# Performance work log

Hardware: AMD Instinct MI355X
Metric: run time of the kernel (lower is better)

## Reference

```python
import jax, jax.numpy as jnp
import numpy as np
from jax import lax

B, H, W = 32, 80, 80
K = 100                        # max_candidates
THRESH = 0.1                   # minutiae_threshold
DIST_T = 16.0
ANGLE_T = np.pi / 6.0
PI = np.pi


def _gauss_kernel1d(ks, sigma):
    c = jnp.arange(ks, dtype=jnp.float32) - ks // 2
    g = jnp.exp(-(c * c) / (2.0 * sigma * sigma))
    return g / g.sum()


def _gaussian_blur(img):  # [B,1,H,W], separable 5x5 sigma=1.5
    k = _gauss_kernel1d(5, 1.5)
    dn = ('NCHW', 'OIHW', 'NCHW')
    x = lax.conv_general_dilated(img, k.reshape(1, 1, 1, 5), (1, 1), [(0, 0), (2, 2)], dimension_numbers=dn)
    x = lax.conv_general_dilated(x, k.reshape(1, 1, 5, 1), (1, 1), [(2, 2), (0, 0)], dimension_numbers=dn)
    return x


def _up8(m):  # nearest-neighbor x8 upsample on last two dims
    return jnp.repeat(jnp.repeat(m, 8, axis=-2), 8, axis=-1)


def _detect_and_nms(score, ori, xoff, yoff):
    # score [H,W]; ori [90,H,W]; xoff/yoff [8,H,W]
    vals, idx = lax.top_k(score.reshape(-1), K)   # sorted descending == argsort by score
    valid = vals > THRESH
    rows = idx // W
    cols = idx % W
    ang_idx = jnp.argmax(ori[:, rows, cols], axis=0)   # [K]
    xo = jnp.argmax(xoff[:, rows, cols], axis=0)
    yo = jnp.argmax(yoff[:, rows, cols], axis=0)
    angles = (ang_idx.astype(jnp.float32) * 2.0 - 89.0) * (PI / 180.0)
    x = cols.astype(jnp.float32) * 8.0 + xo.astype(jnp.float32)
    y = rows.astype(jnp.float32) * 8.0 + yo.astype(jnp.float32)
    mnt = jnp.stack([x, y, angles, vals], axis=-1)     # [K,4]
    # pairwise suppression mask (cdist + circular angle delta)
    d2 = jnp.sum((mnt[:, None, :2] - mnt[None, :, :2]) ** 2, axis=-1)
    dist = jnp.sqrt(d2)
    ad = jnp.abs(angles[:, None] - angles[None, :])
    am = jnp.minimum(ad, 2.0 * PI - ad)
    sup = (dist < DIST_T) & (am < ANGLE_T)
    ar = jnp.arange(K)
    def body(i, keep):
        s = sup[i] & (ar > i)
        return jnp.where(keep[i], keep & ~s, keep)
    keep = lax.fori_loop(0, K, body, valid)
    return mnt, keep


def setup_inputs() -> dict:
    key = jax.random.key(0)
    ks = jax.random.split(key, 7)
    return {
        'segmentation': jax.random.uniform(ks[0], (B, 1, H, W), jnp.float32),
        'minutiae_score': jax.random.uniform(ks[1], (B, 1, H, W), jnp.float32),
        'minutiae_orientation': jax.random.normal(ks[2], (B, 90, H, W), jnp.float32),
        'minutiae_x_offset': jax.random.normal(ks[3], (B, 8, H, W), jnp.float32),
        'minutiae_y_offset': jax.random.normal(ks[4], (B, 8, H, W), jnp.float32),
        'orientation': jax.random.normal(ks[5], (B, 90, H, W), jnp.float32),
        'enhanced_real': jax.random.normal(ks[6], (B, 1, 8 * H, 8 * W), jnp.float32),
    }


def reference(segmentation, minutiae_score, minutiae_orientation,
              minutiae_x_offset, minutiae_y_offset, orientation, enhanced_real):
    # --- segmentation mask: round -> gaussian blur -> round
    cleaned = jnp.round(_gaussian_blur(jnp.round(segmentation[:, 0])[:, None]))[:, 0]  # [B,H,W]
    cleaned_up = _up8(cleaned)                                                          # [B,8H,8W]
    # --- minutiae detection (threshold via masked top-k) + sequential NMS
    score = minutiae_score[:, 0] * cleaned
    mnt, keep = jax.vmap(_detect_and_nms)(score, minutiae_orientation,
                                          minutiae_x_offset, minutiae_y_offset)
    # --- orientation field
    ori_idx = jnp.argmax(orientation, axis=1).astype(jnp.float32)   # [B,H,W]
    ori_field = (_up8(ori_idx) * 2.0 - 89.0) * (PI / 180.0) * cleaned_up
    # --- enhanced image: mask + per-image min-max normalize to [0,255]
    enh = enhanced_real[:, 0] * cleaned_up
    ef = enh.reshape(B, -1)
    emin = jnp.min(ef, axis=1, keepdims=True)
    emax = jnp.max(ef, axis=1, keepdims=True)
    enorm = (ef - emin) / (emax - emin + 1e-8)
    enh_visual = enorm.reshape(B, 8 * H, 8 * W) * 255.0
    return (mnt, keep.astype(jnp.float32), enh_visual, cleaned_up * 255.0, ori_field)
```

## Files before the change

kernel.cpp:

```cpp
#include <hip/hip_runtime.h>
#include <math.h>

#define BN  32
#define H   80
#define W   80
#define HW  6400
#define KC  100
#define NCH 90
#define UW  640
#define UHW 409600

static constexpr size_t OUT_MNT   = 0;
static constexpr size_t OUT_KEEP  = (size_t)BN * KC * 4;
static constexpr size_t OUT_ENH   = OUT_KEEP + (size_t)BN * KC;
static constexpr size_t OUT_CLEAN = OUT_ENH + (size_t)BN * UHW;
static constexpr size_t OUT_ORI   = OUT_CLEAN + (size_t)BN * UHW;

#define PI_F 3.14159265358979323846
#define MM_BLOCKS 64
#define CAP 2048
#define CLEAN_BLOCKS 320
#define ORI_BLOCKS2 400
#define GAT_BLOCKS 800
#define FIN_BLOCKS 12800

typedef float vfloat4 __attribute__((ext_vector_type(4)));

__device__ __forceinline__ unsigned enc_f(float f) {
    unsigned u = __float_as_uint(f);
    return (u & 0x80000000u) ? ~u : (u | 0x80000000u);
}
__device__ __forceinline__ float dec_f(unsigned k) {
    return (k & 0x80000000u) ? __uint_as_float(k ^ 0x80000000u) : __uint_as_float(~k);
}
__device__ __forceinline__ unsigned long long shflx(unsigned long long v, int off) {
    unsigned hi = (unsigned)__shfl_xor((int)(unsigned)(v >> 32), off);
    unsigned lo = (unsigned)__shfl_xor((int)(unsigned)(v & 0xffffffffull), off);
    return ((unsigned long long)hi << 32) | lo;
}

__global__ __launch_bounds__(512) void k_pre(const float* __restrict__ seg,
                                             const float* __restrict__ ori,
                                             float* __restrict__ cleaned_g,
                                             float* __restrict__ ori_idx) {
    __shared__ __align__(16) char um[16384];
    const int bx = blockIdx.x, tid = threadIdx.x;

    if (bx < CLEAN_BLOCKS) {
        float* s_in = (float*)um;
        float* s_h  = (float*)um + 960;
        const int b = bx / 10, band = bx % 10;
        const int r0 = band * 8 - 2;

        float g[5];
        {
            float s = 0.f;
            #pragma unroll
            for (int i = 0; i < 5; i++) {
                float c = (float)(i - 2);
                g[i] = expf(-(c * c) / 4.5f);
                s += g[i];
            }
            #pragma unroll
            for (int i = 0; i < 5; i++) g[i] /= s;
        }

        for (int i = tid; i < 12 * 80; i += 512) {
            int lr = i / 80, w = i % 80;
            int gr = r0 + lr;
            s_in[i] = (gr >= 0 && gr < H) ? rintf(seg[(size_t)b * HW + gr * W + w]) : 0.f;
        }
        __syncthreads();
        for (int i = tid; i < 12 * 80; i += 512) {
            int lr = i / 80, w = i % 80;
            float acc = 0.f;
            #pragma unroll
            for (int dx = -2; dx <= 2; dx++) {
                int ww = w + dx;
                if (ww >= 0 && ww < W) acc += s_in[lr * 80 + ww] * g[dx + 2];
            }
            s_h[i] = acc;
        }
        __syncthreads();
        for (int i = tid; i < 8 * 80; i += 512) {
            int k = i / 80, w = i % 80;
            float acc = 0.f;
            #pragma unroll
            for (int dy = 0; dy < 5; dy++) acc += s_h[(k + dy) * 80 + w] * g[dy];
            cleaned_g[(size_t)b * HW + (band * 8 + k) * W + w] = rintf(acc);
        }
    } else {
        float4* s_bv = (float4*)um;
        float4* s_bj = (float4*)um + 512;
        const int grp = tid >> 7, ln = tid & 127;
        const int p4 = (bx - CLEAN_BLOCKS) * 128 + ln;
        const int b = p4 / (HW / 4), pp = p4 % (HW / 4);
        const float4* o = (const float4*)(ori + (size_t)b * NCH * HW) + pp;
        const int cs = (grp * NCH) >> 2, ce = ((grp + 1) * NCH) >> 2;

        float4 bv = o[(size_t)cs * (HW / 4)];
        float4 bj = make_float4((float)cs, (float)cs, (float)cs, (float)cs);
        for (int j = cs + 1; j < ce; j++) {
            float4 v = o[(size_t)j * (HW / 4)];
            if (v.x > bv.x) { bv.x = v.x; bj.x = (float)j; }
            if (v.y > bv.y) { bv.y = v.y; bj.y = (float)j; }
            if (v.z > bv.z) { bv.z = v.z; bj.z = (float)j; }
            if (v.w > bv.w) { bv.w = v.w; bj.w = (float)j; }
        }
        s_bv[tid] = bv; s_bj[tid] = bj;
        __syncthreads();
        if (grp == 0) {
            #pragma unroll
            for (int g = 1; g < 4; g++) {
                float4 v = s_bv[g * 128 + ln], jx = s_bj[g * 128 + ln];
                if (v.x > bv.x) { bv.x = v.x; bj.x = jx.x; }
                if (v.y > bv.y) { bv.y = v.y; bj.y = jx.y; }
                if (v.z > bv.z) { bv.z = v.z; bj.z = jx.z; }
                if (v.w > bv.w) { bv.w = v.w; bj.w = jx.w; }
            }
            ((float4*)ori_idx)[p4] = bj;
        }
    }
}

__global__ __launch_bounds__(512) void k_mid(const float* __restrict__ mscore,
                                             const float* __restrict__ cleaned,
                                             const float* __restrict__ enh,
                                             float* __restrict__ pmin,
                                             float* __restrict__ pmax,
                                             int* __restrict__ ws_idx,
                                             float* __restrict__ ws_val) {
    __shared__ __align__(16) char um[20480];
    __shared__ unsigned long long s_sel[KC];
    __shared__ unsigned s_rm[HW / 32];
    __shared__ int s_cnt[5];
    __shared__ int s_n;
    __shared__ float s_T;
    __shared__ int s_mode;
    __shared__ float smin[8], smax[8];

    const int bx = blockIdx.x, tid = threadIdx.x;
    const int lane = tid & 63;

    if (bx < BN) {
        unsigned long long* s_cand = (unsigned long long*)um;
        unsigned long long* s_red  = (unsigned long long*)um + CAP;
        const int b = bx;

        if (tid < HW / 32) s_rm[tid] = 0u;
        if (tid < 5) s_cnt[tid] = 0;
        __syncthreads();

        float sc[13];
        #pragma unroll
        for (int j = 0; j < 13; j++) {
            int i = j * 512 + tid;
            sc[j] = (i < HW) ? mscore[(size_t)b * HW + i] * cleaned[(size_t)b * HW + i]
                             : -1.0f;
        }

        int c0 = 0, c1 = 0, c2 = 0, c3 = 0, c4 = 0;
        #pragma unroll
        for (int j = 0; j < 13; j++) {
            float v = sc[j];
            c0 += (v > 0.95f); c1 += (v > 0.9f); c2 += (v > 0.8f);
            c3 += (v > 0.5f);  c4 += (v > 0.0f);
        }
        #pragma unroll
        for (int off = 32; off > 0; off >>= 1) {
            c0 += __shfl_xor(c0, off); c1 += __shfl_xor(c1, off);
            c2 += __shfl_xor(c2, off); c3 += __shfl_xor(c3, off);
            c4 += __shfl_xor(c4, off);
        }
        if (lane == 0) {
            atomicAdd(&s_cnt[0], c0); atomicAdd(&s_cnt[1], c1);
            atomicAdd(&s_cnt[2], c2); atomicAdd(&s_cnt[3], c3);
            atomicAdd(&s_cnt[4], c4);
        }
        __syncthreads();

        if (tid == 0) {
            int n95 = s_cnt[0], n90 = s_cnt[1], n80 = s_cnt[2], n50 = s_cnt[3], n0 = s_cnt[4];
            int mode; float T = 0.f;
            if (n0 < KC)                      { mode = 1; }
            else if (n95 >= KC && n95 <= CAP) { mode = 0; T = 0.95f; }
            else if (n90 >= KC && n90 <= CAP) { mode = 0; T = 0.9f; }
            else if (n80 >= KC && n80 <= CAP) { mode = 0; T = 0.8f; }
            else if (n50 >= KC && n50 <= CAP) { mode = 0; T = 0.5f; }
            else if (n0 <= CAP)               { mode = 0; T = 0.0f; }
            else                              { mode = 2; }
            s_mode = mode; s_T = T; s_n = 0;
        }
        __syncthreads();
        const int mode = s_mode;

        if (mode != 2) {
            const float T = s_T;
            #pragma unroll
            for (int j = 0; j < 13; j++) {
                int i = j * 512 + tid;
                bool take = (mode == 0) ? (sc[j] > T)
                                        : (sc[j] > 0.f || (i < 256 && sc[j] == 0.0f));
                if (take) {
                    int pos = atomicAdd(&s_n, 1);
                    s_cand[pos] = ((unsigned long long)enc_f(sc[j]) << 32) | (unsigned)(HW - i);
                }
            }
            __syncthreads();
            const int n = s_n;
            for (int c = tid; c < n; c += 512) {
                unsigned long long kk = s_cand[c];
                int rank = 0;
                for (int m = 0; m < n; m++) rank += (s_cand[m] > kk) ? 1 : 0;
                if (rank < KC) s_sel[rank] = kk;
            }
            __syncthreads();
        } else {
            for (int k = 0; k < KC; k++) {
                unsigned long long lmax = 0ull;
                #pragma unroll
                for (int j = 0; j < 13; j++) {
                    int i = j * 512 + tid;
                    if (i < HW && sc[j] >= 0.f && !((s_rm[i >> 5] >> (i & 31)) & 1u)) {
                        unsigned long long kk =
                            ((unsigned long long)enc_f(sc[j]) << 32) | (unsigned)(HW - i);
                        if (kk > lmax) lmax = kk;
                    }
                }
                s_red[tid] = lmax;
                __syncthreads();
                for (int off = 256; off > 0; off >>= 1) {
                    if (tid < off) {
                        unsigned long long o = s_red[tid + off];
                        if (o > s_red[tid]) s_red[tid] = o;
                    }
                    __syncthreads();
                }
                if (tid == 0) {
                    unsigned long long wkey = s_red[0];
                    s_sel[k] = wkey;
                    int wi = HW - (int)(wkey & 0xffffffffull);
                    s_rm[wi >> 5] |= 1u << (wi & 31);
                }
                __syncthreads();
            }
        }

        if (tid < KC) {
            unsigned long long e = s_sel[tid];
            ws_idx[(size_t)b * KC + tid] = HW - (int)(e & 0xffffffffull);
            ws_val[(size_t)b * KC + tid] = dec_f((unsigned)(e >> 32));
        }
    } else {
        const int mb = bx - BN;
        const int b = mb >> 6, chunk = mb & 63;
        const float4* e4 = (const float4*)(enh + (size_t)b * UHW);
        const float* cb = cleaned + (size_t)b * HW;

        float vmin = INFINITY, vmax = -INFINITY;
        for (int i = chunk * 512 + tid; i < UHW / 4; i += MM_BLOCKS * 512) {
            float4 v = e4[i];
            int p = i * 4;
            int Y = p / UW, X = p % UW;
            float c = cb[(Y >> 3) * W + (X >> 3)];
            float a = v.x * c, bb = v.y * c, cc = v.z * c, dd = v.w * c;
            vmin = fminf(vmin, fminf(fminf(a, bb), fminf(cc, dd)));
            vmax = fmaxf(vmax, fmaxf(fmaxf(a, bb), fmaxf(cc, dd)));
        }
        #pragma unroll
        for (int off = 32; off > 0; off >>= 1) {
            vmin = fminf(vmin, __shfl_xor(vmin, off));
            vmax = fmaxf(vmax, __shfl_xor(vmax, off));
        }
        int wave = tid >> 6;
        if (lane == 0) { smin[wave] = vmin; smax[wave] = vmax; }
        __syncthreads();
        if (tid == 0) {
            float m0 = smin[0], m1 = smax[0];
            #pragma unroll
            for (int wv = 1; wv < 8; wv++) {
                m0 = fminf(m0, smin[wv]);
                m1 = fmaxf(m1, smax[wv]);
            }
            pmin[b * MM_BLOCKS + chunk] = m0;
            pmax[b * MM_BLOCKS + chunk] = m1;
        }
    }
}

__global__ __launch_bounds__(256) void k_fg(const float* __restrict__ enh,
                                            const float* __restrict__ cleaned,
                                            const float* __restrict__ ori_idx,
                                            const float* __restrict__ pmin,
                                            const float* __restrict__ pmax,
                                            const float* __restrict__ mori,
                                            const float* __restrict__ mxo,
                                            const float* __restrict__ myo,
                                            const int* __restrict__ ws_idx,
                                            const float* __restrict__ ws_val,
                                            float* __restrict__ out) {
    const int bx = blockIdx.x, tid = threadIdx.x;

    if (bx < GAT_BLOCKS) {
        const int lane = tid & 63;
        const int wid = bx * 4 + (tid >> 6);
        const int b = wid / KC, k = wid % KC;
        const int idx = ws_idx[(size_t)b * KC + k];

        const float* pm = mori + (size_t)b * NCH * HW + idx;
        unsigned long long kk =
            ((unsigned long long)enc_f(pm[(size_t)lane * HW]) << 32) | (unsigned)(127 - lane);
        if (lane < NCH - 64) {
            unsigned long long k1 =
                ((unsigned long long)enc_f(pm[(size_t)(64 + lane) * HW]) << 32)
                | (unsigned)(127 - (64 + lane));
            if (k1 > kk) kk = k1;
        }
        unsigned long long kx = 0ull, ky = 0ull;
        if (lane >= 32 && lane < 40)
            kx = ((unsigned long long)enc_f(mxo[((size_t)b * 8 + (lane - 32)) * HW + idx]) << 32)
                 | (unsigned)(15 - (lane - 32));
        if (lane >= 40 && lane < 48)
            ky = ((unsigned long long)enc_f(myo[((size_t)b * 8 + (lane - 40)) * HW + idx]) << 32)
                 | (unsigned)(15 - (lane - 40));

        #pragma unroll
        for (int off = 32; off > 0; off >>= 1) {
            unsigned long long o;
            o = shflx(kk, off); if (o > kk) kk = o;
            o = shflx(kx, off); if (o > kx) kx = o;
            o = shflx(ky, off); if (o > ky) ky = o;
        }

        if (lane == 0) {
            int ch = 127 - (int)(kk & 0xffffffffull);
            int xo = 15  - (int)(kx & 0xffffffffull);
            int yo = 15  - (int)(ky & 0xffffffffull);
            int r = idx / W, c = idx % W;
            float4 m;
            m.x = (float)c * 8.0f + (float)xo;
            m.y = (float)r * 8.0f + (float)yo;
            m.z = ((float)ch * 2.0f - 89.0f) * (float)(PI_F / 180.0);
            m.w = ws_val[(size_t)b * KC + k];
            ((float4*)(out + OUT_MNT))[(size_t)b * KC + k] = m;
        }
    } else {
        __shared__ float s_emin, s_emax;
        const int fb = bx - GAT_BLOCKS;
        const int b = fb / 400;
        if (tid < 64) {
            float vmin = pmin[b * MM_BLOCKS + tid];
            float vmax = pmax[b * MM_BLOCKS + tid];
            #pragma unroll
            for (int off = 32; off > 0; off >>= 1) {
                vmin = fminf(vmin, __shfl_xor(vmin, off));
                vmax = fmaxf(vmax, __shfl_xor(vmax, off));
            }
            if (tid == 0) { s_emin = vmin; s_emax = vmax; }
        }
        __syncthreads();

        int t4 = fb * 256 + tid;
        int p4 = t4 % (UHW / 4);
        int p = p4 * 4;
        int Y = p / UW, X = p % UW;
        int cidx = b * HW + (Y >> 3) * W + (X >> 3);
        float c  = cleaned[cidx];
        float oi = ori_idx[cidx];
        float emin = s_emin, emax = s_emax;
        float inv = 255.0f / (emax - emin + 1e-8f);

        float4 e = ((const float4*)enh)[t4];
        vfloat4 ev;
        ev.x = (e.x * c - emin) * inv;
        ev.y = (e.y * c - emin) * inv;
        ev.z = (e.z * c - emin) * inv;
        ev.w = (e.w * c - emin) * inv;

        float cv = c * 255.0f;
        float ov = (oi * 2.0f - 89.0f) * (float)(PI_F / 180.0) * c;
        vfloat4 cvv = {cv, cv, cv, cv};
        vfloat4 ovv = {ov, ov, ov, ov};

        __builtin_nontemporal_store(ev,  ((vfloat4*)(out + OUT_ENH))   + t4);
        __builtin_nontemporal_store(cvv, ((vfloat4*)(out + OUT_CLEAN)) + t4);
        __builtin_nontemporal_store(ovv, ((vfloat4*)(out + OUT_ORI))   + t4);
    }
}

__global__ __launch_bounds__(64) void k_nms(float* __restrict__ out) {
    const int b = blockIdx.x, l = threadIdx.x;
    const float4* mnt = (const float4*)(out + OUT_MNT) + (size_t)b * KC;
    float4 m0 = mnt[l];
    bool has1 = (l + 64) < KC;
    float4 m1 = has1 ? mnt[l + 64] : make_float4(0.f, 0.f, 0.f, -1.f);
    int keep0 = (m0.w > 0.1f) ? 1 : 0;
    int keep1 = (has1 && m1.w > 0.1f) ? 1 : 0;

    for (int i = 0; i < KC; i++) {
        bool hi = i >= 64;
        int src = i & 63;
        float xi = __shfl(hi ? m1.x : m0.x, src);
        float yi = __shfl(hi ? m1.y : m0.y, src);
        float ai = __shfl(hi ? m1.z : m0.z, src);
        int   ki = __shfl(hi ? keep1 : keep0, src);
        if (ki) {
            if (keep0 && l > i) {
                float dx = xi - m0.x, dy = yi - m0.y;
                float dist = sqrtf(dx * dx + dy * dy);
                float ad = fabsf(ai - m0.z);
                float am = fminf(ad, (float)(2.0 * PI_F) - ad);
                if (dist < 16.0f && am < (float)(PI_F / 6.0)) keep0 = 0;
            }
            if (keep1 && (l + 64) > i) {
                float dx = xi - m1.x, dy = yi - m1.y;
                float dist = sqrtf(dx * dx + dy * dy);
                float ad = fabsf(ai - m1.z);
                float am = fminf(ad, (float)(2.0 * PI_F) - ad);
                if (dist < 16.0f && am < (float)(PI_F / 6.0)) keep1 = 0;
            }
        }
    }
    out[OUT_KEEP + (size_t)b * KC + l] = (float)keep0;
    if (has1) out[OUT_KEEP + (size_t)b * KC + 64 + l] = (float)keep1;
}

extern "C" void kernel_launch(void* const* d_in, const int* in_sizes, int n_in,
                              void* d_out, int out_size, void* d_ws, size_t ws_size,
                              hipStream_t stream) {
    const float* seg    = (const float*)d_in[0];
    const float* mscore = (const float*)d_in[1];
    const float* mori   = (const float*)d_in[2];
    const float* mxo    = (const float*)d_in[3];
    const float* myo    = (const float*)d_in[4];
    const float* ori    = (const float*)d_in[5];
    const float* enh    = (const float*)d_in[6];
    float* out = (float*)d_out;

    float* cleaned = (float*)d_ws;
    float* ori_idx = cleaned + (size_t)BN * HW;
    float* pmin    = ori_idx + (size_t)BN * HW;
    float* pmax    = pmin + (size_t)BN * MM_BLOCKS;
    int*   ws_idx  = (int*)(pmax + (size_t)BN * MM_BLOCKS);
    float* ws_val  = (float*)(ws_idx + (size_t)BN * KC);

    const int nPre = CLEAN_BLOCKS + ORI_BLOCKS2;
    const int nMid = BN + BN * MM_BLOCKS;
    const int nFG  = GAT_BLOCKS + FIN_BLOCKS;

    k_pre<<<nPre, 512, 0, stream>>>(seg, ori, cleaned, ori_idx);
    k_mid<<<nMid, 512, 0, stream>>>(mscore, cleaned, enh, pmin, pmax, ws_idx, ws_val);
    k_fg<<<nFG, 256, 0, stream>>>(enh, cleaned, ori_idx, pmin, pmax,
                                  mori, mxo, myo, ws_idx, ws_val, out);
    k_nms<<<BN, 64, 0, stream>>>(out);
}
```

Measured before the change: 94.07 us.

## Move cleaned/orientation output writes into mid kernel and finalize min/max via last-block

Moves the writes of the upsampled cleaned mask and orientation field out of the final kernel and into the middle kernel as extra blocks. These blocks can then run alongside the serial top-k selection blocks instead of waiting behind them. The per-image min/max reduction is finished by the last arriving block, detected with an atomic counter and threadfence, so the final kernel reads two scalars instead of re-reducing partials. This adds an atomic counter that must be reset each launch, and the middle kernel now launches more blocks.

```diff
diff --git a/kernel.cpp b/kernel.cpp
--- a/kernel.cpp
+++ b/kernel.cpp
@@ -21,8 +21,9 @@
 #define CAP 2048
 #define CLEAN_BLOCKS 320
 #define ORI_BLOCKS2 400
+#define FINA_BLOCKS 6400
 #define GAT_BLOCKS 800
-#define FIN_BLOCKS 12800
+#define FINB_BLOCKS 12800
 
 typedef float vfloat4 __attribute__((ext_vector_type(4)));
 
@@ -42,9 +43,12 @@
 __global__ __launch_bounds__(512) void k_pre(const float* __restrict__ seg,
                                              const float* __restrict__ ori,
                                              float* __restrict__ cleaned_g,
-                                             float* __restrict__ ori_idx) {
+                                             float* __restrict__ ori_idx,
+                                             int* __restrict__ cnt) {
     __shared__ __align__(16) char um[16384];
     const int bx = blockIdx.x, tid = threadIdx.x;
+
+    if (bx == 0 && tid < BN) cnt[tid] = 0;
 
     if (bx < CLEAN_BLOCKS) {
         float* s_in = (float*)um;
@@ -126,10 +130,14 @@
 __global__ __launch_bounds__(512) void k_mid(const float* __restrict__ mscore,
                                              const float* __restrict__ cleaned,
                                              const float* __restrict__ enh,
+                                             const float* __restrict__ ori_idx,
                                              float* __restrict__ pmin,
                                              float* __restrict__ pmax,
+                                             float* __restrict__ mm,
+                                             int* __restrict__ cnt,
                                              int* __restrict__ ws_idx,
-                                             float* __restrict__ ws_val) {
+                                             float* __restrict__ ws_val,
+                                             float* __restrict__ out) {
     __shared__ __align__(16) char um[20480];
     __shared__ unsigned long long s_sel[KC];
     __shared__ unsigned s_rm[HW / 32];
@@ -138,6 +146,7 @@
     __shared__ float s_T;
     __shared__ int s_mode;
     __shared__ float smin[8], smax[8];
+    __shared__ int s_last;
 
     const int bx = blockIdx.x, tid = threadIdx.x;
     const int lane = tid & 63;
@@ -251,7 +260,7 @@
             ws_idx[(size_t)b * KC + tid] = HW - (int)(e & 0xffffffffull);
             ws_val[(size_t)b * KC + tid] = dec_f((unsigned)(e >> 32));
         }
-    } else {
+    } else if (bx < BN + BN * MM_BLOCKS) {
         const int mb = bx - BN;
         const int b = mb >> 6, chunk = mb & 63;
         const float4* e4 = (const float4*)(enh + (size_t)b * UHW);
@@ -284,15 +293,46 @@
             }
             pmin[b * MM_BLOCKS + chunk] = m0;
             pmax[b * MM_BLOCKS + chunk] = m1;
-        }
+            __threadfence();
+            int done = atomicAdd(&cnt[b], 1);
+            s_last = (done == MM_BLOCKS - 1) ? 1 : 0;
+        }
+        __syncthreads();
+        if (s_last) {
+            __threadfence();
+            if (tid < MM_BLOCKS) {
+                float fmin = pmin[b * MM_BLOCKS + tid];
+                float fmax = pmax[b * MM_BLOCKS + tid];
+                #pragma unroll
+                for (int off = 32; off > 0; off >>= 1) {
+                    fmin = fminf(fmin, __shfl_xor(fmin, off));
+                    fmax = fmaxf(fmax, __shfl_xor(fmax, off));
+                }
+                if (tid == 0) { mm[2 * b] = fmin; mm[2 * b + 1] = fmax; }
+            }
+        }
+    } else {
+        const int fb = bx - (BN + BN * MM_BLOCKS);
+        const int t4 = fb * 512 + tid;
+        const int b = t4 / (UHW / 4);
+        const int p4 = t4 % (UHW / 4);
+        const int p = p4 * 4;
+        const int Y = p / UW, X = p % UW;
+        const int cidx = b * HW + (Y >> 3) * W + (X >> 3);
+        const float c  = cleaned[cidx];
+        const float oi = ori_idx[cidx];
+        const float cv = c * 255.0f;
+        const float ov = (oi * 2.0f - 89.0f) * (float)(PI_F / 180.0) * c;
+        vfloat4 cvv = {cv, cv, cv, cv};
+        vfloat4 ovv = {ov, ov, ov, ov};
+        __builtin_nontemporal_store(cvv, ((vfloat4*)(out + OUT_CLEAN)) + t4);
+        __builtin_nontemporal_store(ovv, ((vfloat4*)(out + OUT_ORI))   + t4);
     }
 }
 
 __global__ __launch_bounds__(256) void k_fg(const float* __restrict__ enh,
                                             const float* __restrict__ cleaned,
-                                            const float* __restrict__ ori_idx,
-                                            const float* __restrict__ pmin,
-                                            const float* __restrict__ pmax,
+                                            const float* __restrict__ mm,
                                             const float* __restrict__ mori,
                                             const float* __restrict__ mxo,
                                             const float* __restrict__ myo,
@@ -345,30 +385,17 @@
             ((float4*)(out + OUT_MNT))[(size_t)b * KC + k] = m;
         }
     } else {
-        __shared__ float s_emin, s_emax;
         const int fb = bx - GAT_BLOCKS;
+        const int t4 = fb * 256 + tid;
         const int b = fb / 400;
-        if (tid < 64) {
-            float vmin = pmin[b * MM_BLOCKS + tid];
-            float vmax = pmax[b * MM_BLOCKS + tid];
-            #pragma unroll
-            for (int off = 32; off > 0; off >>= 1) {
-                vmin = fminf(vmin, __shfl_xor(vmin, off));
-                vmax = fmaxf(vmax, __shfl_xor(vmax, off));
-            }
-            if (tid == 0) { s_emin = vmin; s_emax = vmax; }
-        }
-        __syncthreads();
-
-        int t4 = fb * 256 + tid;
-        int p4 = t4 % (UHW / 4);
-        int p = p4 * 4;
-        int Y = p / UW, X = p % UW;
-        int cidx = b * HW + (Y >> 3) * W + (X >> 3);
-        float c  = cleaned[cidx];
-        float oi = ori_idx[cidx];
-        float emin = s_emin, emax = s_emax;
-        float inv = 255.0f / (emax - emin + 1e-8f);
+        const int p4 = t4 % (UHW / 4);
+        const int p = p4 * 4;
+        const int Y = p / UW, X = p % UW;
+        const int cidx = b * HW + (Y >> 3) * W + (X >> 3);
+        const float c = cleaned[cidx];
+        const float emin = mm[2 * b];
+        const float emax = mm[2 * b + 1];
+        const float inv = 255.0f / (emax - emin + 1e-8f);
 
         float4 e = ((const float4*)enh)[t4];
         vfloat4 ev;
@@ -376,15 +403,7 @@
         ev.y = (e.y * c - emin) * inv;
         ev.z = (e.z * c - emin) * inv;
         ev.w = (e.w * c - emin) * inv;
-
-        float cv = c * 255.0f;
-        float ov = (oi * 2.0f - 89.0f) * (float)(PI_F / 180.0) * c;
-        vfloat4 cvv = {cv, cv, cv, cv};
-        vfloat4 ovv = {ov, ov, ov, ov};
-
-        __builtin_nontemporal_store(ev,  ((vfloat4*)(out + OUT_ENH))   + t4);
-        __builtin_nontemporal_store(cvv, ((vfloat4*)(out + OUT_CLEAN)) + t4);
-        __builtin_nontemporal_store(ovv, ((vfloat4*)(out + OUT_ORI))   + t4);
+        __builtin_nontemporal_store(ev, ((vfloat4*)(out + OUT_ENH)) + t4);
     }
 }
 
@@ -441,16 +460,19 @@
     float* ori_idx = cleaned + (size_t)BN * HW;
     float* pmin    = ori_idx + (size_t)BN * HW;
     float* pmax    = pmin + (size_t)BN * MM_BLOCKS;
-    int*   ws_idx  = (int*)(pmax + (size_t)BN * MM_BLOCKS);
+    float* mm      = pmax + (size_t)BN * MM_BLOCKS;
+    int*   ws_idx  = (int*)(mm + 2 * BN);
     float* ws_val  = (float*)(ws_idx + (size_t)BN * KC);
+    int*   cnt     = (int*)(ws_val + (size_t)BN * KC);
 
     const int nPre = CLEAN_BLOCKS + ORI_BLOCKS2;
-    const int nMid = BN + BN * MM_BLOCKS;
-    const int nFG  = GAT_BLOCKS + FIN_BLOCKS;
-
-    k_pre<<<nPre, 512, 0, stream>>>(seg, ori, cleaned, ori_idx);
-    k_mid<<<nMid, 512, 0, stream>>>(mscore, cleaned, enh, pmin, pmax, ws_idx, ws_val);
-    k_fg<<<nFG, 256, 0, stream>>>(enh, cleaned, ori_idx, pmin, pmax,
+    const int nMid = BN + BN * MM_BLOCKS + FINA_BLOCKS;
+    const int nFG  = GAT_BLOCKS + FINB_BLOCKS;
+
+    k_pre<<<nPre, 512, 0, stream>>>(seg, ori, cleaned, ori_idx, cnt);
+    k_mid<<<nMid, 512, 0, stream>>>(mscore, cleaned, enh, ori_idx,
+                                    pmin, pmax, mm, cnt, ws_idx, ws_val, out);
+    k_fg<<<nFG, 256, 0, stream>>>(enh, cleaned, mm,
                                   mori, mxo, myo, ws_idx, ws_val, out);
     k_nms<<<BN, 64, 0, stream>>>(out);
 }
```

After: 190.3 us. 2.02x slower.
